# Kernel tuning notes

Measured on AMD Instinct MI355X. Metric: run time of the kernel, lower is better.

Reference implementation:

```python
import jax, jax.numpy as jnp
import numpy as np

D = 128
H = 8
B = 4
L = 2048


def setup_inputs() -> dict:
    key = jax.random.key(0)
    ks = jax.random.split(key, 5)
    s = 1.0 / np.sqrt(D)
    x = jax.random.normal(ks[0], (B, L, D), dtype=jnp.float32)
    Wq = jax.random.normal(ks[1], (D, D * H), dtype=jnp.float32) * s
    Wk = jax.random.normal(ks[2], (D, D * H), dtype=jnp.float32) * s
    Wv = jax.random.normal(ks[3], (D, D * H), dtype=jnp.float32) * s
    Wu = jax.random.normal(ks[4], (D * H, D), dtype=jnp.float32) * (1.0 / np.sqrt(D * H))
    bu = jnp.zeros((D,), dtype=jnp.float32)
    return {"x": x, "Wq": Wq, "Wk": Wk, "Wv": Wv, "Wu": Wu, "bu": bu}


def reference(x, Wq, Wk, Wv, Wu, bu):
    b, l, d = x.shape
    h = H
    # project and split heads: [b, l, h, d] -> [b, h, l, d]
    q = (x @ Wq).reshape(b, l, h, d).transpose(0, 2, 1, 3)
    k = (x @ Wk).reshape(b, l, h, d).transpose(0, 2, 1, 3)
    v = (x @ Wv).reshape(b, l, h, d).transpose(0, 2, 1, 3)
    scores = jnp.einsum("bhqd,bhkd->bhqk", q, k) / jnp.sqrt(jnp.float32(d))
    w = jax.nn.softmax(scores, axis=-1)
    out = jnp.einsum("bhqk,bhkd->bhqd", w, v)  # [b, h, l, d]
    out = out.transpose(0, 2, 1, 3).reshape(b, l, h * d)
    return out @ Wu + bu
```

## Files before the change

kernel.cpp:

```cpp
#include <hip/hip_runtime.h>
#include <stdint.h>

#define D_ 128
#define H_ 8
#define B_ 4
#define L_ 2048
#define NH (B_*H_)

typedef __bf16 bf16x8 __attribute__((ext_vector_type(8)));
typedef float f32x4 __attribute__((ext_vector_type(4)));
typedef float f32x16 __attribute__((ext_vector_type(16)));
typedef unsigned short u16;
typedef u16 u16x2 __attribute__((ext_vector_type(2)));
typedef u16 u16x4 __attribute__((ext_vector_type(4)));
typedef u16 u16x8 __attribute__((ext_vector_type(8)));
typedef uint32_t u32x2 __attribute__((ext_vector_type(2)));
typedef uint32_t u32x4 __attribute__((ext_vector_type(4)));
typedef float fvec4 __attribute__((ext_vector_type(4)));

__device__ __forceinline__ u16 f2b(float f){
    uint32_t u = __builtin_bit_cast(uint32_t, f);
    u += 0x7fffu + ((u >> 16) & 1u);
    return (u16)(u >> 16);
}
__device__ __forceinline__ u16 f2b_native(float f){
    return __builtin_bit_cast(u16, (__bf16)f);
}
__device__ __forceinline__ uint32_t pk2(float a, float b){
    u16x2 v = { f2b_native(a), f2b_native(b) };
    return __builtin_bit_cast(uint32_t, v);
}
__device__ __forceinline__ float ex2(float x){
#if __has_builtin(__builtin_amdgcn_exp2f)
    return __builtin_amdgcn_exp2f(x);
#else
    return exp2f(x);
#endif
}
__device__ __forceinline__ u32x2 permswap(uint32_t a, uint32_t b){
#if __has_builtin(__builtin_amdgcn_permlane32_swap)
    return __builtin_amdgcn_permlane32_swap(a, b, false, false);
#else
    asm volatile("v_permlane32_swap_b32 %0, %1" : "+v"(a), "+v"(b));
    u32x2 r; r[0] = a; r[1] = b; return r;
#endif
}
__device__ __forceinline__ bf16x8 asbf(u16x8 v){ return __builtin_bit_cast(bf16x8, v); }
#define MFMA(a,b,c)   __builtin_amdgcn_mfma_f32_16x16x32_bf16((a),(b),(c),0,0,0)
#define MFMA32(a,b,c) __builtin_amdgcn_mfma_f32_32x32x16_bf16((a),(b),(c),0,0,0)

__device__ __forceinline__ void gld16(const u16* g, u16* l){
    __builtin_amdgcn_global_load_lds(
        (const __attribute__((address_space(1))) void*)g,
        (__attribute__((address_space(3))) void*)l, 16, 0, 0);
}

__global__ __launch_bounds__(256)
void cvt_all(const float* __restrict__ x, const float* __restrict__ Wq,
             const float* __restrict__ Wk, const float* __restrict__ Wv,
             const float* __restrict__ Wu,
             u16* __restrict__ xb, u16* __restrict__ wT, u16* __restrict__ wuT)
{
    const int blk = blockIdx.x;
    const int t = threadIdx.x;
    if (blk < 512){
        size_t i = ((size_t)blk*256 + t)*8;
        fvec4 lo = *(const fvec4*)&x[i];
        fvec4 hi = *(const fvec4*)&x[i+4];
        u16x8 u;
        for (int j=0;j<4;++j){ u[j]=f2b(lo[j]); u[4+j]=f2b(hi[j]); }
        *(u16x8*)&xb[i] = u;
        return;
    }
    __shared__ __align__(16) u16 T[128][144];
    const int b = blk - 512;
    const float* src; int ld, coff, roff; u16* dst;
    if (b < 24){
        int mat = b>>3, head = b&7;
        src = (mat==0)?Wq:((mat==1)?Wk:Wv); ld = D_*H_; coff = head*128; roff = 0;
        dst = wT + (size_t)b*16384;
    } else {
        src = Wu; ld = D_; coff = 0; roff = (b-24)*128;
        dst = wuT + (size_t)(b-24)*16384;
    }
    for (int it=0; it<16; ++it){
        int k = it*8 + (t>>5), n0 = (t&31)*4;
        fvec4 wv = *(const fvec4*)&src[(size_t)(roff+k)*ld + coff + n0];
        for (int i=0;i<4;++i) T[n0+i][k] = f2b(wv[i]);
    }
    __syncthreads();
    for (int it=0; it<8; ++it){
        int gi = it*256 + t; int n = gi>>4, g = gi&15;
        *(u16x8*)&dst[n*128 + g*8] = *(const u16x8*)&T[n][(g^(n&7))*8];
    }
}

__global__ __launch_bounds__(256)
void qkv_proj(const u16* __restrict__ xb, const u16* __restrict__ wT,
              u16* __restrict__ q_ws, u16* __restrict__ k_ws, u16* __restrict__ v_ws)
{
    const int head = blockIdx.x;
    const int rt   = blockIdx.y;
    const int mat  = blockIdx.z;

    __shared__ __align__(16) u16 Xs[128*128];
    __shared__ __align__(16) u16 Ws[128*128];

    const int t = threadIdx.x;
    const int row0 = rt*128;
    const u16* wsrc = wT + (size_t)(mat*8 + head)*16384;

    for (int it=0; it<8; ++it){
        int gi = it*256 + t;
        int r = gi>>4, g = gi&15;
        gld16(&xb[(size_t)(row0+r)*D_ + ((g ^ (r&7))*8)], &Xs[(it*256 + (t>>6)*64)*8]);
        gld16(&wsrc[gi*8],                                &Ws[(it*256 + (t>>6)*64)*8]);
    }
    asm volatile("s_waitcnt vmcnt(0)" ::: "memory");
    __builtin_amdgcn_s_barrier();

    const int wave = t>>6, lane = t&63;
    const int wr = wave>>1, wc = wave&1;
    const int lrow = lane&15, lgrp = lane>>4;
    const int swz = lrow&7;

    f32x4 acc[4][4] = {};
    #pragma unroll
    for (int kc=0;kc<4;++kc){
        const int gd = kc*4 + lgrp;
        bf16x8 a[4], bfr[4];
        #pragma unroll
        for (int mr=0;mr<4;++mr)
            a[mr] = asbf(*(const u16x8*)&Xs[(wr*64+mr*16+lrow)*128 + ((gd ^ swz)*8)]);
        #pragma unroll
        for (int nr=0;nr<4;++nr)
            bfr[nr] = asbf(*(const u16x8*)&Ws[(wc*64+nr*16+lrow)*128 + ((gd ^ swz)*8)]);
        #pragma unroll
        for (int mr=0;mr<4;++mr)
            #pragma unroll
            for (int nr=0;nr<4;++nr)
                acc[mr][nr] = MFMA(a[mr], bfr[nr], acc[mr][nr]);
    }

    const float qscale = 0.12751879455370425f;
    for (int mr=0;mr<4;++mr){
        for (int nr=0;nr<4;++nr){
            f32x4 v = acc[mr][nr];
            int baserow = row0 + wr*64 + mr*16 + lgrp*4;
            int cd = wc*64 + nr*16 + lrow;
            int b  = baserow / L_;
            int l  = baserow % L_;
            int bh = b*H_ + head;
            if (mat==2){
                u16x4 pv;
                for (int r=0;r<4;++r) pv[r] = f2b(v[r]);
                size_t va = (size_t)bh*D_*L_ + (size_t)(l>>6)*8192 + ((l&63)>>3)*1024 + cd*8 + (l&7);
                *(u16x4*)&v_ws[va] = pv;
            } else if (mat==1){
                for (int r=0;r<4;++r){
                    int l2 = l + r;
                    size_t ka = (size_t)bh*L_*D_ + (size_t)(l2>>6)*8192 + (cd>>3)*512 + (l2&63)*8 + (cd&7);
                    k_ws[ka] = f2b(v[r]);
                }
            } else {
                for (int r=0;r<4;++r)
                    q_ws[((size_t)bh*L_ + (l + r))*D_ + cd] = f2b(v[r]*qscale);
            }
        }
    }
}

__global__ __launch_bounds__(512)
void attn(const u16* __restrict__ q_ws, const u16* __restrict__ k_ws,
          const u16* __restrict__ v_ws, u16* __restrict__ o_ws)
{
    const int wg = ((blockIdx.x & 7) << 5) | (blockIdx.x >> 3);
    const int qt = wg & 7;
    const int bh = wg >> 3;

    const int t = threadIdx.x, wave = t>>6, lane = t&63;
    const int q31 = lane & 31;
    const int hi  = lane >> 5;

    __shared__ __align__(16) u16 Kb[4][64*128];
    __shared__ __align__(16) u16 Vb[4][128*64];

    const int q0 = qt*256 + wave*32;

    bf16x8 qf[8];
    #pragma unroll
    for (int ks=0; ks<8; ++ks)
        qf[ks] = asbf(*(const u16x8*)&q_ws[((size_t)bh*L_ + q0 + q31)*D_ + ks*16 + hi*8]);

    const u16* kp = k_ws + (size_t)bh*L_*D_;
    const u16* vp = v_ws + (size_t)bh*D_*L_;

    auto stage = [&](int buf){
        #pragma unroll
        for (int i=0;i<2;++i){
            gld16(kp + (i*512 + t)*8, &Kb[buf][(i*512 + wave*64)*8]);
            gld16(vp + (i*512 + t)*8, &Vb[buf][(i*512 + wave*64)*8]);
        }
        kp += 8192;
        vp += 8192;
    };

    auto qkt = [&](int buf, f32x16& S0, f32x16& S1){
        f32x16 s0a = {}, s0b = {}, s1a = {}, s1b = {};
        #pragma unroll
        for (int ks=0; ks<4; ++ks){
            const int g0 = ks*2+hi, g1 = (ks+4)*2+hi;
            bf16x8 ka0 = asbf(*(const u16x8*)&Kb[buf][g0*512 + q31*8]);
            bf16x8 ka1 = asbf(*(const u16x8*)&Kb[buf][g1*512 + q31*8]);
            bf16x8 kb0 = asbf(*(const u16x8*)&Kb[buf][g0*512 + (32+q31)*8]);
            bf16x8 kb1 = asbf(*(const u16x8*)&Kb[buf][g1*512 + (32+q31)*8]);
            s0a = MFMA32(ka0, qf[ks],   s0a);
            s0b = MFMA32(ka1, qf[ks+4], s0b);
            s1a = MFMA32(kb0, qf[ks],   s1a);
            s1b = MFMA32(kb1, qf[ks+4], s1b);
        }
        S0 = s0a + s0b;
        S1 = s1a + s1b;
    };

    float lsA = 0.f, lsB = 0.f;
    f32x16 o4[4] = {};

    stage(0);
    stage(1);
    stage(2);
    asm volatile("s_waitcnt vmcnt(4)" ::: "memory");
    __builtin_amdgcn_s_barrier();

    f32x16 sP0, sP1, sN0, sN1;
    qkt(0, sP0, sP1);

    const int NT = L_/64;
    for (int kt=0; kt<NT; ++kt){
        const int cur = kt & 3;
        if (kt < NT-3) stage((kt+3) & 3);

        __builtin_amdgcn_s_setprio(1);
        if (kt < NT-1) qkt((kt+1) & 3, sN0, sN1);
        __builtin_amdgcn_s_setprio(0);

        #define SM_PV(SREG, KS) do { \
            float p0 = ex2(SREG[((KS&1)*8)+0]); \
            float p1 = ex2(SREG[((KS&1)*8)+1]); \
            float p2 = ex2(SREG[((KS&1)*8)+2]); \
            float p3 = ex2(SREG[((KS&1)*8)+3]); \
            float p4 = ex2(SREG[((KS&1)*8)+4]); \
            float p5 = ex2(SREG[((KS&1)*8)+5]); \
            float p6 = ex2(SREG[((KS&1)*8)+6]); \
            float p7 = ex2(SREG[((KS&1)*8)+7]); \
            lsA += (p0+p1)+(p2+p3); \
            lsB += (p4+p5)+(p6+p7); \
            uint32_t cA = pk2(p0,p1), cB = pk2(p2,p3); \
            uint32_t cC = pk2(p4,p5), cD = pk2(p6,p7); \
            u32x2 r0 = permswap(cA, cC); \
            u32x2 r1 = permswap(cB, cD); \
            u32x4 wv; \
            wv[0] = r0[0];  wv[1] = r1[0]; \
            wv[2] = r0[1];  wv[3] = r1[1]; \
            bf16x8 pa = __builtin_bit_cast(bf16x8, wv); \
            __builtin_amdgcn_s_setprio(1); \
            _Pragma("unroll") \
            for (int nc2=0; nc2<4; ++nc2){ \
                bf16x8 vb = asbf(*(const u16x8*)&Vb[cur][ (KS*2+hi)*1024 + (nc2*32+q31)*8 ]); \
                o4[nc2] = MFMA32(pa, vb, o4[nc2]); \
            } \
            __builtin_amdgcn_s_setprio(0); \
        } while(0)

        SM_PV(sP0, 0);
        SM_PV(sP0, 1);
        SM_PV(sP1, 2);
        SM_PV(sP1, 3);
        #undef SM_PV

        if (kt < NT-1){
            if (kt <= NT-4) asm volatile("s_waitcnt vmcnt(4)" ::: "memory");
            else            asm volatile("s_waitcnt vmcnt(0)" ::: "memory");
            __builtin_amdgcn_s_barrier();
        }
        sP0 = sN0;
        sP1 = sN1;
    }

    float lsum = lsA + lsB;
    lsum += __shfl_xor(lsum, 32, 64);
    float inv = 1.0f / lsum;

    const int b = bh / H_, h = bh % H_;
    #pragma unroll
    for (int m=0; m<4; ++m){
        #pragma unroll
        for (int i=0; i<4; ++i){
            const int reg = m*4 + i;
            const int row = i + 8*m + 4*hi;
            float riv = __shfl(inv, row, 64);
            const int l = q0 + row;
            size_t base = ((size_t)(b*L_ + l))*(D_*H_) + h*128 + q31;
            #pragma unroll
            for (int nc2=0; nc2<4; ++nc2)
                o_ws[base + nc2*32] = f2b_native(o4[nc2][reg] * riv);
        }
    }
}

__global__ __launch_bounds__(256)
void out_proj(const u16* __restrict__ o_ws, const u16* __restrict__ wuT,
              const float* __restrict__ bu, float* __restrict__ out)
{
    const int rt = blockIdx.x;
    const int t = threadIdx.x, wave = t>>6, lane = t&63;
    const int wr = wave>>1, wc = wave&1;
    const int lrow = lane&15, lgrp = lane>>4;
    const int swz = lrow&7;

    __shared__ __align__(16) u16 As[2][32*128];
    __shared__ __align__(16) u16 Ws[2][128*128];

    const int row0 = rt*32;
    f32x4 acc[4] = {};

    auto stage = [&](int ks){
        const int buf = ks & 1;
        int gi = t;
        int r = gi>>4, g = gi&15;
        gld16(&o_ws[(size_t)(row0+r)*(D_*H_) + ks*128 + ((g ^ (r&7))*8)], &As[buf][((t>>6)*64)*8]);
        gi = 256 + t;
        r = gi>>4; g = gi&15;
        gld16(&o_ws[(size_t)(row0+r)*(D_*H_) + ks*128 + ((g ^ (r&7))*8)], &As[buf][(256 + (t>>6)*64)*8]);
        const u16* wsrc = wuT + (size_t)ks*16384;
        #pragma unroll
        for (int it=0; it<8; ++it)
            gld16(&wsrc[(it*256 + t)*8], &Ws[buf][(it*256 + (t>>6)*64)*8]);
    };

    stage(0);
    for (int ks=0; ks<8; ++ks){
        const int buf = ks & 1;
        if (ks < 7){
            stage(ks+1);
            asm volatile("s_waitcnt vmcnt(10)" ::: "memory");
        } else {
            asm volatile("s_waitcnt vmcnt(0)" ::: "memory");
        }
        __builtin_amdgcn_s_barrier();

        #pragma unroll
        for (int kc=0;kc<4;++kc){
            const int gd = kc*4 + lgrp;
            bf16x8 a = asbf(*(const u16x8*)&As[buf][(wr*16+lrow)*128 + ((gd ^ swz)*8)]);
            #pragma unroll
            for (int nc=0;nc<4;++nc){
                bf16x8 b = asbf(*(const u16x8*)&Ws[buf][(wc*64+nc*16+lrow)*128 + ((gd ^ swz)*8)]);
                acc[nc] = MFMA(a, b, acc[nc]);
            }
        }
        __builtin_amdgcn_s_barrier();
    }

    for (int nc=0;nc<4;++nc){
        for (int r=0;r<4;++r){
            int row = row0 + wr*16 + lgrp*4 + r;
            int n = wc*64 + nc*16 + lrow;
            out[(size_t)row*D_ + n] = acc[nc][r] + bu[n];
        }
    }
}

extern "C" void kernel_launch(void* const* d_in, const int* in_sizes, int n_in,
                              void* d_out, int out_size, void* d_ws, size_t ws_size,
                              hipStream_t stream)
{
    const float* x  = (const float*)d_in[0];
    const float* Wq = (const float*)d_in[1];
    const float* Wk = (const float*)d_in[2];
    const float* Wv = (const float*)d_in[3];
    const float* Wu = (const float*)d_in[4];
    const float* bu = (const float*)d_in[5];
    float* out = (float*)d_out;

    u16* ws = (u16*)d_ws;
    const size_t SZ = (size_t)NH * L_ * D_;
    u16* q_ws = ws;
    u16* k_ws = q_ws + SZ;
    u16* v_ws = k_ws + SZ;
    u16* o_ws = v_ws + SZ;
    u16* x_bf = o_ws + SZ;
    u16* wT   = x_bf + (size_t)B_*L_*D_;
    u16* wuT  = wT + 24*16384;

    cvt_all<<<dim3(544), 256, 0, stream>>>(x, Wq, Wk, Wv, Wu, x_bf, wT, wuT);
    qkv_proj<<<dim3(H_, (B_*L_)/128, 3), 256, 0, stream>>>(x_bf, wT, q_ws, k_ws, v_ws);
    attn<<<dim3((L_/256)*NH), 512, 0, stream>>>(q_ws, k_ws, v_ws, o_ws);
    out_proj<<<dim3((B_*L_)/32), 256, 0, stream>>>(o_ws, wuT, bu, out);
}
```

Baseline: 120.5 us.

## Restructure attention loop into paired-tile stages with one barrier per pair

Replaces the 4-buffer, 3-ahead K/V prefetch pipeline, which overlapped the next tile's QK^T with the current softmax/PV, with a loop over pairs of 64-key tiles. Each iteration stages the next two tiles, computes QK^T then PV for each tile in sequence, and waits for all loads (vmcnt(0)) plus a barrier once per pair. This halves the number of barriers and drops the register-held next-tile scores. In exchange it loses the QK^T/PV software overlap and shortens the prefetch distance.

New measurement: 119.0 us, median of 4. About the same (-1.2%).

```diff
diff --git a/kernel.cpp b/kernel.cpp
--- a/kernel.cpp
+++ b/kernel.cpp
@@ -228,64 +228,69 @@
 
     stage(0);
     stage(1);
-    stage(2);
-    asm volatile("s_waitcnt vmcnt(4)" ::: "memory");
+    asm volatile("s_waitcnt vmcnt(0)" ::: "memory");
     __builtin_amdgcn_s_barrier();
 
-    f32x16 sP0, sP1, sN0, sN1;
-    qkt(0, sP0, sP1);
-
-    const int NT = L_/64;
-    for (int kt=0; kt<NT; ++kt){
-        const int cur = kt & 3;
-        if (kt < NT-3) stage((kt+3) & 3);
-
+    #define SM_PV(SREG, KS, BUF) do { \
+        float p0 = ex2(SREG[((KS&1)*8)+0]); \
+        float p1 = ex2(SREG[((KS&1)*8)+1]); \
+        float p2 = ex2(SREG[((KS&1)*8)+2]); \
+        float p3 = ex2(SREG[((KS&1)*8)+3]); \
+        float p4 = ex2(SREG[((KS&1)*8)+4]); \
+        float p5 = ex2(SREG[((KS&1)*8)+5]); \
+        float p6 = ex2(SREG[((KS&1)*8)+6]); \
+        float p7 = ex2(SREG[((KS&1)*8)+7]); \
+        lsA += (p0+p1)+(p2+p3); \
+        lsB += (p4+p5)+(p6+p7); \
+        uint32_t cA = pk2(p0,p1), cB = pk2(p2,p3); \
+        uint32_t cC = pk2(p4,p5), cD = pk2(p6,p7); \
+        u32x2 r0 = permswap(cA, cC); \
+        u32x2 r1 = permswap(cB, cD); \
+        u32x4 wv; \
+        wv[0] = r0[0];  wv[1] = r1[0]; \
+        wv[2] = r0[1];  wv[3] = r1[1]; \
+        bf16x8 pa = __builtin_bit_cast(bf16x8, wv); \
+        __builtin_amdgcn_s_setprio(1); \
+        _Pragma("unroll") \
+        for (int nc2=0; nc2<4; ++nc2){ \
+            bf16x8 vb = asbf(*(const u16x8*)&Vb[BUF][ (KS*2+hi)*1024 + (nc2*32+q31)*8 ]); \
+            o4[nc2] = MFMA32(pa, vb, o4[nc2]); \
+        } \
+        __builtin_amdgcn_s_setprio(0); \
+    } while(0)
+
+    const int NJ = L_/128;
+    for (int j=0; j<NJ; ++j){
+        const int sa = (2*j) & 3, sb = (2*j+1) & 3;
+        if (j < NJ-1){
+            stage((2*j+2) & 3);
+            stage((2*j+3) & 3);
+        }
+
+        f32x16 sA0, sA1;
         __builtin_amdgcn_s_setprio(1);
-        if (kt < NT-1) qkt((kt+1) & 3, sN0, sN1);
+        qkt(sa, sA0, sA1);
         __builtin_amdgcn_s_setprio(0);
-
-        #define SM_PV(SREG, KS) do { \
-            float p0 = ex2(SREG[((KS&1)*8)+0]); \
-            float p1 = ex2(SREG[((KS&1)*8)+1]); \
-            float p2 = ex2(SREG[((KS&1)*8)+2]); \
-            float p3 = ex2(SREG[((KS&1)*8)+3]); \
-            float p4 = ex2(SREG[((KS&1)*8)+4]); \
-            float p5 = ex2(SREG[((KS&1)*8)+5]); \
-            float p6 = ex2(SREG[((KS&1)*8)+6]); \
-            float p7 = ex2(SREG[((KS&1)*8)+7]); \
-            lsA += (p0+p1)+(p2+p3); \
-            lsB += (p4+p5)+(p6+p7); \
-            uint32_t cA = pk2(p0,p1), cB = pk2(p2,p3); \
-            uint32_t cC = pk2(p4,p5), cD = pk2(p6,p7); \
-            u32x2 r0 = permswap(cA, cC); \
-            u32x2 r1 = permswap(cB, cD); \
-            u32x4 wv; \
-            wv[0] = r0[0];  wv[1] = r1[0]; \
-            wv[2] = r0[1];  wv[3] = r1[1]; \
-            bf16x8 pa = __builtin_bit_cast(bf16x8, wv); \
-            __builtin_amdgcn_s_setprio(1); \
-            _Pragma("unroll") \
-            for (int nc2=0; nc2<4; ++nc2){ \
-                bf16x8 vb = asbf(*(const u16x8*)&Vb[cur][ (KS*2+hi)*1024 + (nc2*32+q31)*8 ]); \
-                o4[nc2] = MFMA32(pa, vb, o4[nc2]); \
-            } \
-            __builtin_amdgcn_s_setprio(0); \
-        } while(0)
-
-        SM_PV(sP0, 0);
-        SM_PV(sP0, 1);
-        SM_PV(sP1, 2);
-        SM_PV(sP1, 3);
-        #undef SM_PV
-
-        if (kt < NT-1){
-            if (kt <= NT-4) asm volatile("s_waitcnt vmcnt(4)" ::: "memory");
-            else            asm volatile("s_waitcnt vmcnt(0)" ::: "memory");
+        SM_PV(sA0, 0, sa);
+        SM_PV(sA0, 1, sa);
+        SM_PV(sA1, 2, sa);
+        SM_PV(sA1, 3, sa);
+
+        f32x16 sB0, sB1;
+        __builtin_amdgcn_s_setprio(1);
+        qkt(sb, sB0, sB1);
+        __builtin_amdgcn_s_setprio(0);
+        SM_PV(sB0, 0, sb);
+        SM_PV(sB0, 1, sb);
+        SM_PV(sB1, 2, sb);
+        SM_PV(sB1, 3, sb);
+
+        if (j < NJ-1){
+            asm volatile("s_waitcnt vmcnt(0)" ::: "memory");
             __builtin_amdgcn_s_barrier();
         }
-        sP0 = sN0;
-        sP1 = sN1;
-    }
+    }
+    #undef SM_PV
 
     float lsum = lsA + lsB;
     lsum += __shfl_xor(lsum, 32, 64);
```
